# Kernel tuning notes

Hardware: AMD Instinct MI355X
Metric: run time of the kernel (lower is better)

## Reference

```python
import jax, jax.numpy as jnp
import numpy as np

GROUPS = 8
EPS = 1e-5
NUM_HEADS = 8


def group_norm(x, gamma, beta):
    # x: [B, C, N]; GroupNorm over (C//G, N) per group, per sample (torch semantics)
    B, C, N = x.shape
    xg = x.reshape(B, GROUPS, (C // GROUPS) * N)
    mean = xg.mean(axis=-1, keepdims=True)
    var = xg.var(axis=-1, keepdims=True)
    xn = ((xg - mean) * jax.lax.rsqrt(var + EPS)).reshape(B, C, N)
    return xn * gamma[None, :, None] + beta[None, :, None]


def setup_inputs() -> dict:
    key = jax.random.key(0)
    ks = jax.random.split(key, 6)
    B, N, C = 4, 2048, 512
    s = 0.02
    return {
        "x": jax.random.normal(ks[0], (B, N, C), jnp.float32),
        "pe": jax.random.normal(ks[1], (B, N, C), jnp.float32),
        "qkv_w": jax.random.normal(ks[2], (3 * C, C), jnp.float32) * s,
        "proj_w": jax.random.normal(ks[3], (C, C), jnp.float32) * s,
        "proj_b": jnp.zeros((C,), jnp.float32),
        "conv1_w": jax.random.normal(ks[4], (C, C), jnp.float32) * s,
        "conv1_b": jnp.zeros((C,), jnp.float32),
        "gn1_g": jnp.ones((C,), jnp.float32),
        "gn1_b": jnp.zeros((C,), jnp.float32),
        "conv2_w": jax.random.normal(ks[5], (C, C), jnp.float32) * s,
        "conv2_b": jnp.zeros((C,), jnp.float32),
        "gn2_g": jnp.ones((C,), jnp.float32),
        "gn2_b": jnp.zeros((C,), jnp.float32),
    }


def reference(x, pe, qkv_w, proj_w, proj_b, conv1_w, conv1_b, gn1_g, gn1_b,
              conv2_w, conv2_b, gn2_g, gn2_b):
    B, N, C = x.shape
    H = NUM_HEADS
    D = C // H
    scale = D ** -0.5

    pe_t = pe.transpose(0, 2, 1)  # [B, C, N]
    # Conv1d(kernel=1) == per-position linear over channels
    p1 = group_norm(jnp.einsum('oc,bcn->bon', conv1_w, pe_t) + conv1_b[None, :, None], gn1_g, gn1_b)
    p2 = group_norm(jnp.einsum('oc,bcn->bon', conv2_w, pe_t) + conv2_b[None, :, None], gn2_g, gn2_b)
    pe_1 = p1.transpose(0, 2, 1)                 # [B, N, C]
    pe_attn = jax.nn.sigmoid(jnp.einsum('bnc,bcm->bnm', pe_1, p2))  # [B, N, N]

    qkv = (x @ qkv_w.T).reshape(B, N, 3, H, D).transpose(2, 0, 3, 1, 4)  # [3, B, H, N, D]
    q, k, v = qkv[0], qkv[1], qkv[2]

    attn = jnp.einsum('bhnd,bhmd->bhnm', q, k) * scale
    attn = attn * pe_attn[:, None, :, :]
    attn = jax.nn.softmax(attn, axis=-1)

    out = jnp.einsum('bhnm,bhmd->bhnd', attn, v)          # [B, H, N, D]
    out = out.transpose(0, 2, 1, 3).reshape(B, N, C)
    return out @ proj_w.T + proj_b
```

## Files before the change

### kernel.cpp

```cpp
#include <hip/hip_runtime.h>
#include <hip/hip_bf16.h>

typedef __attribute__((ext_vector_type(8))) short bf16x8;
typedef __attribute__((ext_vector_type(4))) float f32x4;

__device__ __forceinline__ float bfu2f(unsigned int u) {
    return __uint_as_float(u << 16);
}
__device__ __forceinline__ unsigned short f2bfu(float f) {
    unsigned int u = __float_as_uint(f);
    u += 0x7fffu + ((u >> 16) & 1u);
    return (unsigned short)(u >> 16);
}

__global__ __launch_bounds__(256) void cvt_f32_bf16(const float* __restrict__ src,
                                                    unsigned short* __restrict__ dst, int n4) {
    int i = blockIdx.x * 256 + threadIdx.x;
    const int stride = gridDim.x * 256;
    for (; i < n4; i += stride) {
        float4 v = reinterpret_cast<const float4*>(src)[i];
        ushort4 o;
        o.x = f2bfu(v.x); o.y = f2bfu(v.y); o.z = f2bfu(v.z); o.w = f2bfu(v.w);
        reinterpret_cast<ushort4*>(dst)[i] = o;
    }
}

template <int EPI>
__global__ __launch_bounds__(256) void gemm_nt(
    const unsigned short* __restrict__ A, const unsigned short* __restrict__ B,
    void* __restrict__ C0, void* __restrict__ C1, void* __restrict__ C2,
    const float* __restrict__ bias, int K, long sA, long sB, long sC) {
    __shared__ unsigned short As[128 * 40];
    __shared__ unsigned short Bs[128 * 40];
    const int tid = threadIdx.x;
    const int l = tid & 63, w = tid >> 6;
    const int wr = w >> 1, wc = w & 1, lr = l & 15, lh = l >> 4;
    const int m0 = blockIdx.y * 128, n0 = blockIdx.x * 128;
    A += (size_t)blockIdx.z * sA;
    B += (size_t)blockIdx.z * sB;
    f32x4 acc[4][4] = {};
    const int rowS = tid >> 2, partS = tid & 3;

    for (int k0 = 0; k0 < K; k0 += 32) {
        *reinterpret_cast<uint4*>(&As[rowS * 40 + partS * 8]) =
            *reinterpret_cast<const uint4*>(A + (size_t)(m0 + rowS) * K + k0 + partS * 8);
        *reinterpret_cast<uint4*>(&As[(rowS + 64) * 40 + partS * 8]) =
            *reinterpret_cast<const uint4*>(A + (size_t)(m0 + rowS + 64) * K + k0 + partS * 8);
        *reinterpret_cast<uint4*>(&Bs[rowS * 40 + partS * 8]) =
            *reinterpret_cast<const uint4*>(B + (size_t)(n0 + rowS) * K + k0 + partS * 8);
        *reinterpret_cast<uint4*>(&Bs[(rowS + 64) * 40 + partS * 8]) =
            *reinterpret_cast<const uint4*>(B + (size_t)(n0 + rowS + 64) * K + k0 + partS * 8);
        __syncthreads();
        bf16x8 af[4], bfr[4];
#pragma unroll
        for (int i = 0; i < 4; i++)
            af[i] = *reinterpret_cast<const bf16x8*>(&As[(wr * 64 + i * 16 + lr) * 40 + lh * 8]);
#pragma unroll
        for (int i = 0; i < 4; i++)
            bfr[i] = *reinterpret_cast<const bf16x8*>(&Bs[(wc * 64 + i * 16 + lr) * 40 + lh * 8]);
#pragma unroll
        for (int mi = 0; mi < 4; mi++)
#pragma unroll
            for (int ni = 0; ni < 4; ni++)
                acc[mi][ni] = __builtin_amdgcn_mfma_f32_16x16x32_bf16(af[mi], bfr[ni], acc[mi][ni], 0, 0, 0);
        __syncthreads();
    }

#pragma unroll
    for (int mi = 0; mi < 4; mi++) {
#pragma unroll
        for (int ni = 0; ni < 4; ni++) {
#pragma unroll
            for (int r = 0; r < 4; r++) {
                const int row = m0 + wr * 64 + mi * 16 + lh * 4 + r;
                const int col = n0 + wc * 64 + ni * 16 + lr;
                float v = acc[mi][ni][r];
                if constexpr (EPI == 0) {
                    v += bias[col];
                    ((unsigned short*)C0)[(size_t)row * 512 + col] = f2bfu(v);
                } else if constexpr (EPI == 1) {
                    const int part = col >> 9, hh = (col >> 6) & 7, d = col & 63;
                    const int b = row >> 11, n = row & 2047;
                    const size_t bh = (size_t)(b * 8 + hh);
                    if (part == 0)
                        ((unsigned short*)C0)[(bh * 2048 + n) * 64 + d] = f2bfu(v * 0.1803368801111244f);
                    else if (part == 1)
                        ((unsigned short*)C1)[(bh * 2048 + n) * 64 + d] = f2bfu(v);
                    else
                        ((unsigned short*)C2)[(bh * 64 + d) * 2048 + n] = f2bfu(v);
                } else if constexpr (EPI == 2) {
                    const float sg = 1.0f / (1.0f + __expf(-v));
                    ((unsigned short*)C0)[(size_t)blockIdx.z * sC + (size_t)row * 2048 + col] = f2bfu(sg);
                } else {
                    ((float*)C0)[(size_t)row * 512 + col] = v + bias[col];
                }
            }
        }
    }
}

__global__ __launch_bounds__(256) void gn_stats_part(const unsigned short* __restrict__ c1,
                                                     const unsigned short* __restrict__ c2,
                                                     float* __restrict__ part) {
    const int bgc = blockIdx.x;
    const int b = bgc >> 6, g = (bgc >> 3) & 7, ch = bgc & 7;
    const int tid = threadIdx.x;
    const size_t base = ((size_t)b * 2048 + ch * 256) * 512 + g * 64;
    float s1 = 0.f, q1 = 0.f, s2 = 0.f, q2 = 0.f;
    for (int c = tid; c < 2048; c += 256) {
        const int n = c >> 3, i8 = (c & 7) * 8;
        const size_t off = base + (size_t)n * 512 + i8;
        uint4 v1 = *reinterpret_cast<const uint4*>(c1 + off);
        uint4 v2 = *reinterpret_cast<const uint4*>(c2 + off);
        unsigned int a1[4] = {v1.x, v1.y, v1.z, v1.w};
        unsigned int a2[4] = {v2.x, v2.y, v2.z, v2.w};
#pragma unroll
        for (int j = 0; j < 4; j++) {
            float x0 = bfu2f(a1[j] & 0xffffu), x1 = bfu2f(a1[j] >> 16);
            s1 += x0 + x1; q1 += x0 * x0 + x1 * x1;
            float y0 = bfu2f(a2[j] & 0xffffu), y1 = bfu2f(a2[j] >> 16);
            s2 += y0 + y1; q2 += y0 * y0 + y1 * y1;
        }
    }
#pragma unroll
    for (int off = 32; off >= 1; off >>= 1) {
        s1 += __shfl_down(s1, off); q1 += __shfl_down(q1, off);
        s2 += __shfl_down(s2, off); q2 += __shfl_down(q2, off);
    }
    __shared__ float red[4][4];
    if ((tid & 63) == 0) {
        const int wv = tid >> 6;
        red[0][wv] = s1; red[1][wv] = q1; red[2][wv] = s2; red[3][wv] = q2;
    }
    __syncthreads();
    if (tid == 0) {
        part[bgc * 4 + 0] = red[0][0] + red[0][1] + red[0][2] + red[0][3];
        part[bgc * 4 + 1] = red[1][0] + red[1][1] + red[1][2] + red[1][3];
        part[bgc * 4 + 2] = red[2][0] + red[2][1] + red[2][2] + red[2][3];
        part[bgc * 4 + 3] = red[3][0] + red[3][1] + red[3][2] + red[3][3];
    }
}

__global__ __launch_bounds__(64) void gn_finish(const float* __restrict__ part,
                                                float* __restrict__ stats) {
    const int t = threadIdx.x;
    if (t < 32) {
        float S1 = 0.f, Q1 = 0.f, S2 = 0.f, Q2 = 0.f;
        for (int ch = 0; ch < 8; ch++) {
            const float* p = part + ((t << 3) + ch) * 4;
            S1 += p[0]; Q1 += p[1]; S2 += p[2]; Q2 += p[3];
        }
        const float inv = 1.0f / 131072.0f;
        float m1 = S1 * inv, m2 = S2 * inv;
        float v1 = fmaxf(Q1 * inv - m1 * m1, 0.f);
        float v2 = fmaxf(Q2 * inv - m2 * m2, 0.f);
        stats[t * 4 + 0] = m1;
        stats[t * 4 + 1] = rsqrtf(v1 + 1e-5f);
        stats[t * 4 + 2] = m2;
        stats[t * 4 + 3] = rsqrtf(v2 + 1e-5f);
    }
}

__global__ __launch_bounds__(256) void gn_apply(unsigned short* __restrict__ c1,
                                                unsigned short* __restrict__ c2,
                                                const float* __restrict__ stats,
                                                const float* __restrict__ g1, const float* __restrict__ b1,
                                                const float* __restrict__ g2, const float* __restrict__ b2) {
    int i = blockIdx.x * 256 + threadIdx.x;
    const int stride = gridDim.x * 256;
    for (; i < 524288; i += stride) {
        const size_t e = (size_t)i * 8;
        const int b = (int)(e >> 20);
        const int o = (int)(e & 511);
        const int g = o >> 6;
        const float* st = stats + ((b << 3) + g) * 4;
        const float m1 = st[0], r1 = st[1], m2 = st[2], r2 = st[3];
        uint4 v1 = *reinterpret_cast<const uint4*>(c1 + e);
        uint4 v2 = *reinterpret_cast<const uint4*>(c2 + e);
        unsigned int a1[4] = {v1.x, v1.y, v1.z, v1.w};
        unsigned int a2[4] = {v2.x, v2.y, v2.z, v2.w};
        unsigned int o1[4], o2[4];
#pragma unroll
        for (int j = 0; j < 4; j++) {
            const int oo = o + j * 2;
            float x0 = (bfu2f(a1[j] & 0xffffu) - m1) * r1 * g1[oo] + b1[oo];
            float x1 = (bfu2f(a1[j] >> 16) - m1) * r1 * g1[oo + 1] + b1[oo + 1];
            o1[j] = (unsigned int)f2bfu(x0) | ((unsigned int)f2bfu(x1) << 16);
            float y0 = (bfu2f(a2[j] & 0xffffu) - m2) * r2 * g2[oo] + b2[oo];
            float y1 = (bfu2f(a2[j] >> 16) - m2) * r2 * g2[oo + 1] + b2[oo + 1];
            o2[j] = (unsigned int)f2bfu(y0) | ((unsigned int)f2bfu(y1) << 16);
        }
        uint4 w1; w1.x = o1[0]; w1.y = o1[1]; w1.z = o1[2]; w1.w = o1[3];
        uint4 w2; w2.x = o2[0]; w2.y = o2[1]; w2.z = o2[2]; w2.w = o2[3];
        *reinterpret_cast<uint4*>(c1 + e) = w1;
        *reinterpret_cast<uint4*>(c2 + e) = w2;
    }
}

__global__ __launch_bounds__(256, 3) void attn_fused(
    const unsigned short* __restrict__ qb, const unsigned short* __restrict__ kb,
    const unsigned short* __restrict__ vT, const unsigned short* __restrict__ pea,
    unsigned short* __restrict__ hbuf) {
    __shared__ unsigned short Ks[2][64 * 64];
    __shared__ unsigned short Vs[2][64 * 64];
    __shared__ unsigned short Pe[64 * 64];
    __shared__ unsigned short Pl[4][16 * 72];
    const int tid = threadIdx.x, l = tid & 63, w = tid >> 6;
    const int lr = l & 15, lh = l >> 4;
    const int bid = blockIdx.x;
    const int h = bid >> 7, rst = bid & 127, nt = rst & 31, b = rst >> 5;
    const size_t bh = (size_t)(b * 8 + h);
    const unsigned short* qp = qb + bh * 2048 * 64;
    const unsigned short* kp = kb + bh * 2048 * 64;
    const unsigned short* vp = vT + bh * 64 * 2048;
    const unsigned short* pep = pea + (size_t)b * 2048 * 2048;
    const int n0 = nt * 64;

    bf16x8 qf[2];
    qf[0] = *reinterpret_cast<const bf16x8*>(qp + (size_t)(n0 + 16 * w + lr) * 64 + lh * 8);
    qf[1] = *reinterpret_cast<const bf16x8*>(qp + (size_t)(n0 + 16 * w + lr) * 64 + 32 + lh * 8);

    const int swz = (lr & 7) << 4;
    const int colK0 = ((16 * lh) ^ swz) >> 1;
    const int colK1 = ((64 + 16 * lh) ^ swz) >> 1;
    const int perow = (16 * w + lr) * 64;
    int peoff[4];
#pragma unroll
    for (int mf = 0; mf < 4; mf++)
        peoff[mf] = perow + (((mf * 2 + (lh >> 1)) ^ (lr & 7)) << 3) + ((lh & 1) << 2);

    f32x4 oacc[4] = {};
    float mrun = -1e30f, lrun = 0.f;

    const int srow = l >> 3, sslot = l & 7;
    auto stage_kv = [&](int bufi, int m0) {
#pragma unroll
        for (int i = 0; i < 2; i++) {
            const int row = w * 16 + i * 8 + srow;
            const int cs = (sslot ^ (row & 7)) * 8;
            const int ldsoff = (w * 16 + i * 8) * 64;
            __builtin_amdgcn_global_load_lds(
                (const __attribute__((address_space(1))) void*)(kp + (size_t)(m0 + row) * 64 + cs),
                (__attribute__((address_space(3))) void*)&Ks[bufi][ldsoff], 16, 0, 0);
            __builtin_amdgcn_global_load_lds(
                (const __attribute__((address_space(1))) void*)(vp + (size_t)row * 2048 + m0 + cs),
                (__attribute__((address_space(3))) void*)&Vs[bufi][ldsoff], 16, 0, 0);
        }
    };
    auto stage_pe = [&](int m0) {
#pragma unroll
        for (int i = 0; i < 2; i++) {
            const int row = w * 16 + i * 8 + srow;
            const int cs = (sslot ^ (row & 7)) * 8;
            const int ldsoff = (w * 16 + i * 8) * 64;
            __builtin_amdgcn_global_load_lds(
                (const __attribute__((address_space(1))) void*)(pep + (size_t)(n0 + row) * 2048 + m0 + cs),
                (__attribute__((address_space(3))) void*)&Pe[ldsoff], 16, 0, 0);
        }
    };

    stage_kv(0, 0);
    stage_pe(0);
    asm volatile("s_waitcnt vmcnt(0)" ::: "memory");
    __syncthreads();

    for (int mt = 0; mt < 32; mt++) {
        const int cur = mt & 1;
        if (mt + 1 < 32) stage_kv(cur ^ 1, (mt + 1) * 64);
        const unsigned short* Kb = Ks[cur];
        const unsigned short* Vb = Vs[cur];

        f32x4 st[4] = {};
        __builtin_amdgcn_s_setprio(1);
#pragma unroll
        for (int mf = 0; mf < 4; mf++) {
            bf16x8 kf0 = *reinterpret_cast<const bf16x8*>(&Kb[(mf * 16 + lr) * 64 + colK0]);
            bf16x8 kf1 = *reinterpret_cast<const bf16x8*>(&Kb[(mf * 16 + lr) * 64 + colK1]);
            st[mf] = __builtin_amdgcn_mfma_f32_16x16x32_bf16(kf0, qf[0], st[mf], 0, 0, 0);
            st[mf] = __builtin_amdgcn_mfma_f32_16x16x32_bf16(kf1, qf[1], st[mf], 0, 0, 0);
        }
        __builtin_amdgcn_s_setprio(0);
        float p[4][4];
#pragma unroll
        for (int mf = 0; mf < 4; mf++) {
            const uint2 pv = *reinterpret_cast<const uint2*>(&Pe[peoff[mf]]);
            p[mf][0] = st[mf][0] * bfu2f(pv.x & 0xffffu);
            p[mf][1] = st[mf][1] * bfu2f(pv.x >> 16);
            p[mf][2] = st[mf][2] * bfu2f(pv.y & 0xffffu);
            p[mf][3] = st[mf][3] * bfu2f(pv.y >> 16);
        }
        __syncthreads();
        if (mt + 1 < 32) stage_pe((mt + 1) * 64);
        float pm = fmaxf(p[0][0], p[0][1]);
        pm = fmaxf(fmaxf(pm, p[0][2]), p[0][3]);
#pragma unroll
        for (int mf = 1; mf < 4; mf++) {
            pm = fmaxf(fmaxf(pm, p[mf][0]), p[mf][1]);
            pm = fmaxf(fmaxf(pm, p[mf][2]), p[mf][3]);
        }
        pm = fmaxf(pm, __shfl_xor(pm, 16));
        pm = fmaxf(pm, __shfl_xor(pm, 32));
        if (__any(pm > mrun + 11.5416f)) {
            const float mnew = fmaxf(mrun, pm);
            const float fac = __builtin_amdgcn_exp2f(mrun - mnew);
            lrun *= fac;
#pragma unroll
            for (int df = 0; df < 4; df++)
#pragma unroll
                for (int r = 0; r < 4; r++) oacc[df][r] *= fac;
            mrun = mnew;
        }
        float ss = 0.f;
        unsigned int pk[8];
#pragma unroll
        for (int mf = 0; mf < 4; mf++) {
#pragma unroll
            for (int t = 0; t < 2; t++) {
                const float a = __builtin_amdgcn_exp2f(p[mf][2 * t] - mrun);
                const float c = __builtin_amdgcn_exp2f(p[mf][2 * t + 1] - mrun);
                unsigned int pkv;
                asm("v_cvt_pk_bf16_f32 %0, %1, %2" : "=v"(pkv) : "v"(a), "v"(c));
                pk[mf * 2 + t] = pkv;
                ss += a + c;
            }
        }
        ss += __shfl_xor(ss, 16);
        ss += __shfl_xor(ss, 32);
        lrun += ss;
#pragma unroll
        for (int mf = 0; mf < 4; mf++)
#pragma unroll
            for (int t = 0; t < 2; t++)
                *reinterpret_cast<unsigned int*>(&Pl[w][lr * 72 + mf * 16 + lh * 4 + 2 * t]) = pk[mf * 2 + t];
        bf16x8 pb0 = *reinterpret_cast<const bf16x8*>(&Pl[w][lr * 72 + lh * 8]);
        bf16x8 pb1 = *reinterpret_cast<const bf16x8*>(&Pl[w][lr * 72 + 32 + lh * 8]);
        __builtin_amdgcn_s_setprio(1);
#pragma unroll
        for (int df = 0; df < 4; df++) {
            bf16x8 vf0 = *reinterpret_cast<const bf16x8*>(&Vb[(df * 16 + lr) * 64 + colK0]);
            bf16x8 vf1 = *reinterpret_cast<const bf16x8*>(&Vb[(df * 16 + lr) * 64 + colK1]);
            oacc[df] = __builtin_amdgcn_mfma_f32_16x16x32_bf16(vf0, pb0, oacc[df], 0, 0, 0);
            oacc[df] = __builtin_amdgcn_mfma_f32_16x16x32_bf16(vf1, pb1, oacc[df], 0, 0, 0);
        }
        __builtin_amdgcn_s_setprio(0);
        if (mt + 1 < 32) {
            asm volatile("s_waitcnt vmcnt(0)" ::: "memory");
            __syncthreads();
        }
    }
    const float inv = 1.0f / lrun;
    const size_t base = ((size_t)b * 2048 + n0 + 16 * w + lr) * 512 + h * 64;
#pragma unroll
    for (int df = 0; df < 4; df++) {
#pragma unroll
        for (int t = 0; t < 2; t++) {
            const unsigned int ua = f2bfu(oacc[df][2 * t] * inv);
            const unsigned int uc = f2bfu(oacc[df][2 * t + 1] * inv);
            *reinterpret_cast<unsigned int*>(&hbuf[base + 16 * df + 4 * lh + 2 * t]) = ua | (uc << 16);
        }
    }
}

extern "C" void kernel_launch(void* const* d_in, const int* in_sizes, int n_in,
                              void* d_out, int out_size, void* d_ws, size_t ws_size,
                              hipStream_t stream) {
    const float* x       = (const float*)d_in[0];
    const float* pe      = (const float*)d_in[1];
    const float* qkv_w   = (const float*)d_in[2];
    const float* proj_w  = (const float*)d_in[3];
    const float* proj_b  = (const float*)d_in[4];
    const float* conv1_w = (const float*)d_in[5];
    const float* conv1_b = (const float*)d_in[6];
    const float* gn1_g   = (const float*)d_in[7];
    const float* gn1_b   = (const float*)d_in[8];
    const float* conv2_w = (const float*)d_in[9];
    const float* conv2_b = (const float*)d_in[10];
    const float* gn2_g   = (const float*)d_in[11];
    const float* gn2_b   = (const float*)d_in[12];
    float* out = (float*)d_out;

    char* ws = (char*)d_ws;
    size_t off = 0;
    auto alloc = [&](size_t bytes) -> void* {
        void* p = ws + off;
        off += (bytes + 255) & ~(size_t)255;
        return p;
    };
    unsigned short* xb     = (unsigned short*)alloc(8388608);
    unsigned short* peb    = (unsigned short*)alloc(8388608);
    unsigned short* qkvwb  = (unsigned short*)alloc(1572864);
    unsigned short* projwb = (unsigned short*)alloc(524288);
    unsigned short* w1b    = (unsigned short*)alloc(524288);
    unsigned short* w2b    = (unsigned short*)alloc(524288);
    unsigned short* c1b    = (unsigned short*)alloc(8388608);
    unsigned short* c2b    = (unsigned short*)alloc(8388608);
    unsigned short* qbuf   = (unsigned short*)alloc(8388608);
    unsigned short* kbuf   = (unsigned short*)alloc(8388608);
    unsigned short* vtb    = (unsigned short*)alloc(8388608);
    unsigned short* peatt  = (unsigned short*)alloc(33554432);
    unsigned short* hbuf   = (unsigned short*)alloc(8388608);
    float* stats           = (float*)alloc(512);
    float* part            = (float*)alloc(4096);

    dim3 blk(256);
    cvt_f32_bf16<<<1024, blk, 0, stream>>>(x, xb, 1048576);
    cvt_f32_bf16<<<1024, blk, 0, stream>>>(pe, peb, 1048576);
    cvt_f32_bf16<<<256, blk, 0, stream>>>(qkv_w, qkvwb, 196608);
    cvt_f32_bf16<<<128, blk, 0, stream>>>(proj_w, projwb, 65536);
    cvt_f32_bf16<<<128, blk, 0, stream>>>(conv1_w, w1b, 65536);
    cvt_f32_bf16<<<128, blk, 0, stream>>>(conv2_w, w2b, 65536);

    gemm_nt<0><<<dim3(4, 64, 1), blk, 0, stream>>>(peb, w1b, c1b, nullptr, nullptr, conv1_b, 512, 0, 0, 0);
    gemm_nt<0><<<dim3(4, 64, 1), blk, 0, stream>>>(peb, w2b, c2b, nullptr, nullptr, conv2_b, 512, 0, 0, 0);
    gn_stats_part<<<256, blk, 0, stream>>>(c1b, c2b, part);
    gn_finish<<<1, 64, 0, stream>>>(part, stats);
    gn_apply<<<1024, blk, 0, stream>>>(c1b, c2b, stats, gn1_g, gn1_b, gn2_g, gn2_b);
    gemm_nt<1><<<dim3(12, 64, 1), blk, 0, stream>>>(xb, qkvwb, qbuf, kbuf, vtb, nullptr, 512, 0, 0, 0);
    gemm_nt<2><<<dim3(16, 16, 4), blk, 0, stream>>>(c1b, c2b, peatt, nullptr, nullptr, nullptr, 512,
                                                    1048576, 1048576, 4194304);
    attn_fused<<<dim3(1024, 1, 1), blk, 0, stream>>>(qbuf, kbuf, vtb, peatt, hbuf);
    gemm_nt<3><<<dim3(4, 64, 1), blk, 0, stream>>>(hbuf, projwb, out, nullptr, nullptr, proj_b, 512, 0, 0, 0);
}
```

Measured before the change: 265.0 us.

## Load pe_attn into registers, reuse K buffer for P, merge conversion and GN kernels

The attention kernel no longer stages the pe_attn tile through LDS. Each lane now loads its own fragment straight into registers, prefetched one tile ahead. The P staging area reuses the current K buffer with a swizzle, which frees LDS so occupancy can rise to 4 blocks per CU, and the syncthreads calls become explicit barriers. Separately, the six f32-to-bf16 conversion launches collapse into two, and gn_finish is folded into gn_apply so every block recomputes the 32 group stats. Together this trims launch overhead and LDS traffic, at the cost of uncoalesced 8-byte global loads for pe_attn and a correctness risk from reusing Ks after the QK step.

```diff
diff --git a/kernel.cpp b/kernel.cpp
--- a/kernel.cpp
+++ b/kernel.cpp
@@ -13,15 +13,38 @@
     return (unsigned short)(u >> 16);
 }
 
-__global__ __launch_bounds__(256) void cvt_f32_bf16(const float* __restrict__ src,
-                                                    unsigned short* __restrict__ dst, int n4) {
+__global__ __launch_bounds__(256) void cvt2(const float* __restrict__ s0, unsigned short* __restrict__ d0,
+                                            const float* __restrict__ s1, unsigned short* __restrict__ d1) {
     int i = blockIdx.x * 256 + threadIdx.x;
     const int stride = gridDim.x * 256;
-    for (; i < n4; i += stride) {
-        float4 v = reinterpret_cast<const float4*>(src)[i];
+    for (; i < 1048576; i += stride) {
+        float4 v = reinterpret_cast<const float4*>(s0)[i];
         ushort4 o;
         o.x = f2bfu(v.x); o.y = f2bfu(v.y); o.z = f2bfu(v.z); o.w = f2bfu(v.w);
-        reinterpret_cast<ushort4*>(dst)[i] = o;
+        reinterpret_cast<ushort4*>(d0)[i] = o;
+        float4 u = reinterpret_cast<const float4*>(s1)[i];
+        ushort4 p;
+        p.x = f2bfu(u.x); p.y = f2bfu(u.y); p.z = f2bfu(u.z); p.w = f2bfu(u.w);
+        reinterpret_cast<ushort4*>(d1)[i] = p;
+    }
+}
+
+__global__ __launch_bounds__(256) void cvtw(const float* __restrict__ s0, unsigned short* __restrict__ d0,
+                                            const float* __restrict__ s1, unsigned short* __restrict__ d1,
+                                            const float* __restrict__ s2, unsigned short* __restrict__ d2,
+                                            const float* __restrict__ s3, unsigned short* __restrict__ d3) {
+    int i = blockIdx.x * 256 + threadIdx.x;
+    const int stride = gridDim.x * 256;
+    for (; i < 393216; i += stride) {
+        const float* s; unsigned short* d; int j;
+        if (i < 196608)      { s = s0; d = d0; j = i; }
+        else if (i < 262144) { s = s1; d = d1; j = i - 196608; }
+        else if (i < 327680) { s = s2; d = d2; j = i - 262144; }
+        else                 { s = s3; d = d3; j = i - 327680; }
+        float4 v = reinterpret_cast<const float4*>(s)[j];
+        ushort4 o;
+        o.x = f2bfu(v.x); o.y = f2bfu(v.y); o.z = f2bfu(v.z); o.w = f2bfu(v.w);
+        reinterpret_cast<ushort4*>(d)[j] = o;
     }
 }
 
@@ -141,39 +164,37 @@
     }
 }
 
-__global__ __launch_bounds__(64) void gn_finish(const float* __restrict__ part,
-                                                float* __restrict__ stats) {
-    const int t = threadIdx.x;
-    if (t < 32) {
+__global__ __launch_bounds__(256) void gn_apply(unsigned short* __restrict__ c1,
+                                                unsigned short* __restrict__ c2,
+                                                const float* __restrict__ part,
+                                                const float* __restrict__ g1, const float* __restrict__ b1,
+                                                const float* __restrict__ g2, const float* __restrict__ b2) {
+    __shared__ float sst[32][4];
+    const int tid = threadIdx.x;
+    if (tid < 32) {
         float S1 = 0.f, Q1 = 0.f, S2 = 0.f, Q2 = 0.f;
         for (int ch = 0; ch < 8; ch++) {
-            const float* p = part + ((t << 3) + ch) * 4;
+            const float* p = part + ((tid << 3) + ch) * 4;
             S1 += p[0]; Q1 += p[1]; S2 += p[2]; Q2 += p[3];
         }
         const float inv = 1.0f / 131072.0f;
         float m1 = S1 * inv, m2 = S2 * inv;
         float v1 = fmaxf(Q1 * inv - m1 * m1, 0.f);
         float v2 = fmaxf(Q2 * inv - m2 * m2, 0.f);
-        stats[t * 4 + 0] = m1;
-        stats[t * 4 + 1] = rsqrtf(v1 + 1e-5f);
-        stats[t * 4 + 2] = m2;
-        stats[t * 4 + 3] = rsqrtf(v2 + 1e-5f);
-    }
-}
-
-__global__ __launch_bounds__(256) void gn_apply(unsigned short* __restrict__ c1,
-                                                unsigned short* __restrict__ c2,
-                                                const float* __restrict__ stats,
-                                                const float* __restrict__ g1, const float* __restrict__ b1,
-                                                const float* __restrict__ g2, const float* __restrict__ b2) {
-    int i = blockIdx.x * 256 + threadIdx.x;
+        sst[tid][0] = m1;
+        sst[tid][1] = rsqrtf(v1 + 1e-5f);
+        sst[tid][2] = m2;
+        sst[tid][3] = rsqrtf(v2 + 1e-5f);
+    }
+    __syncthreads();
+    int i = blockIdx.x * 256 + tid;
     const int stride = gridDim.x * 256;
     for (; i < 524288; i += stride) {
         const size_t e = (size_t)i * 8;
         const int b = (int)(e >> 20);
         const int o = (int)(e & 511);
         const int g = o >> 6;
-        const float* st = stats + ((b << 3) + g) * 4;
+        const float* st = sst[(b << 3) + g];
         const float m1 = st[0], r1 = st[1], m2 = st[2], r2 = st[3];
         uint4 v1 = *reinterpret_cast<const uint4*>(c1 + e);
         uint4 v2 = *reinterpret_cast<const uint4*>(c2 + e);
@@ -197,14 +218,12 @@
     }
 }
 
-__global__ __launch_bounds__(256, 3) void attn_fused(
+__global__ __launch_bounds__(256, 4) void attn_fused(
     const unsigned short* __restrict__ qb, const unsigned short* __restrict__ kb,
     const unsigned short* __restrict__ vT, const unsigned short* __restrict__ pea,
     unsigned short* __restrict__ hbuf) {
     __shared__ unsigned short Ks[2][64 * 64];
     __shared__ unsigned short Vs[2][64 * 64];
-    __shared__ unsigned short Pe[64 * 64];
-    __shared__ unsigned short Pl[4][16 * 72];
     const int tid = threadIdx.x, l = tid & 63, w = tid >> 6;
     const int lr = l & 15, lh = l >> 4;
     const int bid = blockIdx.x;
@@ -223,11 +242,12 @@
     const int swz = (lr & 7) << 4;
     const int colK0 = ((16 * lh) ^ swz) >> 1;
     const int colK1 = ((64 + 16 * lh) ^ swz) >> 1;
-    const int perow = (16 * w + lr) * 64;
-    int peoff[4];
+
+    const unsigned short* perp = pep + (size_t)(n0 + 16 * w + lr) * 2048;
+    uint2 peR[4];
 #pragma unroll
     for (int mf = 0; mf < 4; mf++)
-        peoff[mf] = perow + (((mf * 2 + (lh >> 1)) ^ (lr & 7)) << 3) + ((lh & 1) << 2);
+        peR[mf] = *reinterpret_cast<const uint2*>(perp + 16 * mf + 4 * lh);
 
     f32x4 oacc[4] = {};
     float mrun = -1e30f, lrun = 0.f;
@@ -247,22 +267,11 @@
                 (__attribute__((address_space(3))) void*)&Vs[bufi][ldsoff], 16, 0, 0);
         }
     };
-    auto stage_pe = [&](int m0) {
-#pragma unroll
-        for (int i = 0; i < 2; i++) {
-            const int row = w * 16 + i * 8 + srow;
-            const int cs = (sslot ^ (row & 7)) * 8;
-            const int ldsoff = (w * 16 + i * 8) * 64;
-            __builtin_amdgcn_global_load_lds(
-                (const __attribute__((address_space(1))) void*)(pep + (size_t)(n0 + row) * 2048 + m0 + cs),
-                (__attribute__((address_space(3))) void*)&Pe[ldsoff], 16, 0, 0);
-        }
-    };
 
     stage_kv(0, 0);
-    stage_pe(0);
     asm volatile("s_waitcnt vmcnt(0)" ::: "memory");
-    __syncthreads();
+    __builtin_amdgcn_s_barrier();
+    __builtin_amdgcn_sched_barrier(0);
 
     for (int mt = 0; mt < 32; mt++) {
         const int cur = mt & 1;
@@ -280,17 +289,25 @@
             st[mf] = __builtin_amdgcn_mfma_f32_16x16x32_bf16(kf1, qf[1], st[mf], 0, 0, 0);
         }
         __builtin_amdgcn_s_setprio(0);
+        asm volatile("s_waitcnt lgkmcnt(0)" ::: "memory");
+        __builtin_amdgcn_s_barrier();
+        __builtin_amdgcn_sched_barrier(0);
+
         float p[4][4];
 #pragma unroll
         for (int mf = 0; mf < 4; mf++) {
-            const uint2 pv = *reinterpret_cast<const uint2*>(&Pe[peoff[mf]]);
-            p[mf][0] = st[mf][0] * bfu2f(pv.x & 0xffffu);
-            p[mf][1] = st[mf][1] * bfu2f(pv.x >> 16);
-            p[mf][2] = st[mf][2] * bfu2f(pv.y & 0xffffu);
-            p[mf][3] = st[mf][3] * bfu2f(pv.y >> 16);
-        }
-        __syncthreads();
-        if (mt + 1 < 32) stage_pe((mt + 1) * 64);
+            p[mf][0] = st[mf][0] * bfu2f(peR[mf].x & 0xffffu);
+            p[mf][1] = st[mf][1] * bfu2f(peR[mf].x >> 16);
+            p[mf][2] = st[mf][2] * bfu2f(peR[mf].y & 0xffffu);
+            p[mf][3] = st[mf][3] * bfu2f(peR[mf].y >> 16);
+        }
+        uint2 peN[4];
+        if (mt + 1 < 32) {
+            const unsigned short* pn = perp + (mt + 1) * 64;
+#pragma unroll
+            for (int mf = 0; mf < 4; mf++)
+                peN[mf] = *reinterpret_cast<const uint2*>(pn + 16 * mf + 4 * lh);
+        }
         float pm = fmaxf(p[0][0], p[0][1]);
         pm = fmaxf(fmaxf(pm, p[0][2]), p[0][3]);
 #pragma unroll
@@ -327,13 +344,17 @@
         ss += __shfl_xor(ss, 16);
         ss += __shfl_xor(ss, 32);
         lrun += ss;
+        unsigned short* PlW = &Ks[cur][w * 1024];
+        const int plswz = (lr & 7) << 4;
 #pragma unroll
         for (int mf = 0; mf < 4; mf++)
 #pragma unroll
-            for (int t = 0; t < 2; t++)
-                *reinterpret_cast<unsigned int*>(&Pl[w][lr * 72 + mf * 16 + lh * 4 + 2 * t]) = pk[mf * 2 + t];
-        bf16x8 pb0 = *reinterpret_cast<const bf16x8*>(&Pl[w][lr * 72 + lh * 8]);
-        bf16x8 pb1 = *reinterpret_cast<const bf16x8*>(&Pl[w][lr * 72 + 32 + lh * 8]);
+            for (int t = 0; t < 2; t++) {
+                const int cb = (mf * 32 + lh * 8 + 4 * t) ^ plswz;
+                *reinterpret_cast<unsigned int*>(&PlW[lr * 64 + (cb >> 1)]) = pk[mf * 2 + t];
+            }
+        bf16x8 pb0 = *reinterpret_cast<const bf16x8*>(&PlW[lr * 64 + (((lh * 16) ^ plswz) >> 1)]);
+        bf16x8 pb1 = *reinterpret_cast<const bf16x8*>(&PlW[lr * 64 + (((64 + lh * 16) ^ plswz) >> 1)]);
         __builtin_amdgcn_s_setprio(1);
 #pragma unroll
         for (int df = 0; df < 4; df++) {
@@ -344,8 +365,11 @@
         }
         __builtin_amdgcn_s_setprio(0);
         if (mt + 1 < 32) {
-            asm volatile("s_waitcnt vmcnt(0)" ::: "memory");
-            __syncthreads();
+            asm volatile("s_waitcnt vmcnt(0) lgkmcnt(0)" ::: "memory");
+            __builtin_amdgcn_s_barrier();
+            __builtin_amdgcn_sched_barrier(0);
+#pragma unroll
+            for (int mf = 0; mf < 4; mf++) peR[mf] = peN[mf];
         }
     }
     const float inv = 1.0f / lrun;
@@ -399,22 +423,16 @@
     unsigned short* vtb    = (unsigned short*)alloc(8388608);
     unsigned short* peatt  = (unsigned short*)alloc(33554432);
     unsigned short* hbuf   = (unsigned short*)alloc(8388608);
-    float* stats           = (float*)alloc(512);
     float* part            = (float*)alloc(4096);
 
     dim3 blk(256);
-    cvt_f32_bf16<<<1024, blk, 0, stream>>>(x, xb, 1048576);
-    cvt_f32_bf16<<<1024, blk, 0, stream>>>(pe, peb, 1048576);
-    cvt_f32_bf16<<<256, blk, 0, stream>>>(qkv_w, qkvwb, 196608);
-    cvt_f32_bf16<<<128, blk, 0, stream>>>(proj_w, projwb, 65536);
-    cvt_f32_bf16<<<128, blk, 0, stream>>>(conv1_w, w1b, 65536);
-    cvt_f32_bf16<<<128, blk, 0, stream>>>(conv2_w, w2b, 65536);
+    cvt2<<<1024, blk, 0, stream>>>(x, xb, pe, peb);
+    cvtw<<<512, blk, 0, stream>>>(qkv_w, qkvwb, proj_w, projwb, conv1_w, w1b, conv2_w, w2b);
 
     gemm_nt<0><<<dim3(4, 64, 1), blk, 0, stream>>>(peb, w1b, c1b, nullptr, nullptr, conv1_b, 512, 0, 0, 0);
     gemm_nt<0><<<dim3(4, 64, 1), blk, 0, stream>>>(peb, w2b, c2b, nullptr, nullptr, conv2_b, 512, 0, 0, 0);
     gn_stats_part<<<256, blk, 0, stream>>>(c1b, c2b, part);
-    gn_finish<<<1, 64, 0, stream>>>(part, stats);
-    gn_apply<<<1024, blk, 0, stream>>>(c1b, c2b, stats, gn1_g, gn1_b, gn2_g, gn2_b);
+    gn_apply<<<1024, blk, 0, stream>>>(c1b, c2b, part, gn1_g, gn1_b, gn2_g, gn2_b);
     gemm_nt<1><<<dim3(12, 64, 1), blk, 0, stream>>>(xb, qkvwb, qbuf, kbuf, vtb, nullptr, 512, 0, 0, 0);
     gemm_nt<2><<<dim3(16, 16, 4), blk, 0, stream>>>(c1b, c2b, peatt, nullptr, nullptr, nullptr, 512,
                                                     1048576, 1048576, 4194304);
```

Result: faster. 250.4 us (-5.5%).
